# Performance work log

Measured on AMD Instinct MI355X. Metric: run time of the kernel, lower is better.

## Reference

```python
import jax, jax.numpy as jnp
import numpy as np

LNF, PNF, H = 128, 128, 128
THRESH = 10.0
NORM = 100.0
EPS = 1e-8


def _linear(x, W, b):
    return x @ W + b


def _glorot(key, shape):
    fan_in = shape[0]
    return jax.random.normal(key, shape, dtype=jnp.float32) / jnp.sqrt(jnp.float32(fan_in))


def setup_inputs() -> dict:
    key = jax.random.key(0)
    ks = jax.random.split(key, 20)
    bs, nl, npr = 4, 128, 1024
    inp = {
        "h_ligand": jax.random.normal(ks[0], (bs, nl, LNF), jnp.float32),
        "x_ligand": jax.random.normal(ks[1], (bs, nl, 3), jnp.float32) * 4.0,
        "h_protein": jax.random.normal(ks[2], (bs, npr, PNF), jnp.float32),
        "x_protein": jax.random.normal(ks[3], (bs, npr, 3), jnp.float32) * 4.0,
        "ligand_mask": jnp.ones((bs, nl, 1), jnp.float32),
        "protein_mask": jnp.ones((bs, npr, 1), jnp.float32),
        # attention MLP: (lnf+pnf+1)->H->H->1
        "aW1": _glorot(ks[4], (LNF + PNF + 1, H)), "ab1": jnp.zeros((H,), jnp.float32),
        "aW2": _glorot(ks[5], (H, H)),            "ab2": jnp.zeros((H,), jnp.float32),
        "aW3": _glorot(ks[6], (H, 1)),            "ab3": jnp.zeros((1,), jnp.float32),
        # value MLP: (pnf+1)->H->lnf
        "vW1": _glorot(ks[7], (PNF + 1, H)),      "vb1": jnp.zeros((H,), jnp.float32),
        "vW2": _glorot(ks[8], (H, LNF)),          "vb2": jnp.zeros((LNF,), jnp.float32),
        # coord MLP: (lnf+pnf+1)->H->1
        "cW1": _glorot(ks[9], (LNF + PNF + 1, H)), "cb1": jnp.zeros((H,), jnp.float32),
        "cW2": _glorot(ks[10], (H, 1)),           "cb2": jnp.zeros((1,), jnp.float32),
    }
    return inp


def reference(h_ligand, x_ligand, h_protein, x_protein, ligand_mask, protein_mask,
              aW1, ab1, aW2, ab2, aW3, ab3, vW1, vb1, vW2, vb2, cW1, cb1, cW2, cb2):
    bs, nl, lnf = h_ligand.shape
    npr = h_protein.shape[1]
    # pairwise geometry [bs, nl, np, ...]
    rel = x_ligand[:, :, None, :] - x_protein[:, None, :, :]
    ds = jnp.sum(rel * rel, axis=-1, keepdims=True)           # dist^2
    dist = jnp.sqrt(ds + EPS)
    edge = (dist < THRESH).astype(h_ligand.dtype)             # radius edge mask
    direction = rel / (dist + EPS)
    hl = jnp.broadcast_to(h_ligand[:, :, None, :], (bs, nl, npr, lnf))
    hp = jnp.broadcast_to(h_protein[:, None, :, :], (bs, nl, npr, h_protein.shape[-1]))
    pm = protein_mask[:, None, :, :]                          # [bs,1,np,1]

    pair_in = jnp.concatenate([hl, hp, ds], axis=-1)
    # attention MLP -> sigmoid
    a = jax.nn.silu(_linear(pair_in, aW1, ab1))
    a = jax.nn.silu(_linear(a, aW2, ab2))
    attn = jax.nn.sigmoid(_linear(a, aW3, ab3)) * pm
    # value MLP
    v = jax.nn.silu(_linear(jnp.concatenate([hp, ds], axis=-1), vW1, vb1))
    val = _linear(v, vW2, vb2)
    # feature messages, masked radius aggregation
    h_cross = jnp.sum(attn * val * edge, axis=2) / NORM       # [bs,nl,lnf]
    # coord MLP -> tanh
    c = jax.nn.silu(_linear(pair_in, cW1, cb1))
    cw = jnp.tanh(_linear(c, cW2, cb2)) * pm
    x_cross = jnp.sum(direction * cw * edge, axis=2) / NORM   # [bs,nl,3]

    h_cross = h_cross * ligand_mask
    x_cross = x_cross * ligand_mask
    return h_cross, x_cross
```

## Files before the change

kernel.cpp:

```cpp
#include <hip/hip_runtime.h>
#include <hip/hip_bf16.h>
#include <math.h>

#define HF 128
#define NL 128
#define NP 1024
#define NB 4
#define EPSF 1e-8f

typedef short bf16x8 __attribute__((ext_vector_type(8)));
typedef float f32x4 __attribute__((ext_vector_type(4)));

__device__ __forceinline__ float fast_rcp(float x){ return __builtin_amdgcn_rcpf(x); }
__device__ __forceinline__ float silu_f(float x){ return x*fast_rcp(1.f+__expf(-x)); }
__device__ __forceinline__ float sigmoid_f(float x){ return fast_rcp(1.f+__expf(-x)); }
__device__ __forceinline__ float tanh_f(float x){ return 1.f - 2.f*fast_rcp(1.f+__expf(2.f*x)); }
__device__ __forceinline__ unsigned short f2bf(float f){ __hip_bfloat16 h=__float2bfloat16(f); return *(unsigned short*)&h; }
__device__ __forceinline__ float bf2f(short u){ unsigned int x = ((unsigned int)(unsigned short)u)<<16; float r; __builtin_memcpy(&r,&x,4); return r; }

__global__ __launch_bounds__(128) void precompute_kernel(
    const float* __restrict__ h_ligand, const float* __restrict__ h_protein,
    const float* __restrict__ aW1, const float* __restrict__ ab1,
    const float* __restrict__ vW1, const float* __restrict__ vb1,
    const float* __restrict__ cW1, const float* __restrict__ cb1,
    const float* __restrict__ aW2, const float* __restrict__ vW2,
    float* __restrict__ Al, float* __restrict__ Cl,
    unsigned short* __restrict__ Ap, unsigned short* __restrict__ Vp,
    unsigned short* __restrict__ Cp,
    unsigned short* __restrict__ WaT, unsigned short* __restrict__ WvT)
{
    const int blk = blockIdx.x, n = threadIdx.x;
    if (blk < 64) {
        __shared__ float rows[8][HF];
        const int r0 = blk*8;
        for (int idx=n; idx<8*HF; idx+=128) rows[idx>>7][idx&127] = h_ligand[r0*HF+idx];
        __syncthreads();
        float aA[8], aC[8];
        const float bA = ab1[n], bC = cb1[n];
        #pragma unroll
        for (int r=0;r<8;++r){ aA[r]=bA; aC[r]=bC; }
        #pragma unroll 4
        for (int k=0;k<HF;++k){
            float wA = aW1[k*HF+n], wC = cW1[k*HF+n];
            #pragma unroll
            for (int r=0;r<8;++r){ aA[r]=fmaf(rows[r][k],wA,aA[r]); aC[r]=fmaf(rows[r][k],wC,aC[r]); }
        }
        #pragma unroll
        for (int r=0;r<8;++r){ Al[(r0+r)*HF+n]=aA[r]; Cl[(r0+r)*HF+n]=aC[r]; }
    } else if (blk < 576) {
        __shared__ float rows[8][HF];
        const int r0 = (blk-64)*8;
        for (int idx=n; idx<8*HF; idx+=128) rows[idx>>7][idx&127] = h_protein[r0*HF+idx];
        __syncthreads();
        float aA[8], aV[8], aC[8];
        const float bV = vb1[n];
        #pragma unroll
        for (int r=0;r<8;++r){ aA[r]=0.f; aV[r]=bV; aC[r]=0.f; }
        #pragma unroll 2
        for (int k=0;k<HF;++k){
            float wA = aW1[(HF+k)*HF+n], wV = vW1[k*HF+n], wC = cW1[(HF+k)*HF+n];
            #pragma unroll
            for (int r=0;r<8;++r){
                float h = rows[r][k];
                aA[r]=fmaf(h,wA,aA[r]); aV[r]=fmaf(h,wV,aV[r]); aC[r]=fmaf(h,wC,aC[r]);
            }
        }
        #pragma unroll
        for (int r=0;r<8;++r){
            Ap[(r0+r)*HF+n]=f2bf(aA[r]); Vp[(r0+r)*HF+n]=f2bf(aV[r]); Cp[(r0+r)*HF+n]=f2bf(aC[r]);
        }
    } else {
        const int m = blk - 576;
        const float* W = (m<8) ? aW2 : vW2;
        unsigned short* WT = (m<8) ? WaT : WvT;
        const int n0 = (m&7)*16;
        #pragma unroll
        for (int kb=0; kb<16; ++kb) {
            int k = kb*8 + (n>>4);
            int col = n0 + (n&15);
            WT[col*HF + k] = f2bf(W[k*HF + col]);
        }
    }
}

__global__ __launch_bounds__(256,2) void egnn_main_kernel(
    const float* __restrict__ x_ligand, const float* __restrict__ x_protein,
    const float* __restrict__ ligand_mask, const float* __restrict__ protein_mask,
    const float* __restrict__ aW1, const float* __restrict__ ab2,
    const float* __restrict__ aW3, const float* __restrict__ ab3,
    const float* __restrict__ vW1, const float* __restrict__ vb2,
    const float* __restrict__ cW1, const float* __restrict__ cW2, const float* __restrict__ cb2,
    const float* __restrict__ Al, const float* __restrict__ Cl,
    const unsigned short* __restrict__ Ap, const unsigned short* __restrict__ Vp,
    const unsigned short* __restrict__ Cp,
    const unsigned short* __restrict__ WaT, const unsigned short* __restrict__ WvT,
    float* __restrict__ out)
{
    __shared__ __align__(16) char smem[50176];
    float* ds_all = (float*)(smem + 32768);
    float* pme    = (float*)(smem + 34816);
    float* dirx   = (float*)(smem + 36864);
    float* diry   = (float*)(smem + 38912);
    float* dirz   = (float*)(smem + 40960);
    unsigned short* jlist = (unsigned short*)(smem + 43008);
    float* Al_s   = (float*)(smem + 44032);
    float* Cl_s   = (float*)(smem + 44544);
    float* aw1l   = (float*)(smem + 45056);
    float* cw1l   = (float*)(smem + 45568);
    float* vw1l   = (float*)(smem + 46080);
    float* cW2s   = (float*)(smem + 46592);
    float* attn_part = (float*)(smem + 47104);
    float* attn_e = (float*)(smem + 47360);
    float* hred   = (float*)(smem + 47616);
    float* xw     = (float*)(smem + 48640);
    int* nact_p   = (int*)(smem + 48704);

    const int t = threadIdx.x, lane = t&63, w = t>>6;
    const int wj = w>>1, wn = w&1;
    const int lr = lane&15, lg = lane>>4;
    const int bi = blockIdx.x;
    const int half = bi & 1;
    const int ii = bi >> 1;
    const int b = ii >> 7;
    const int jbase = half*512;

    const float xl0 = x_ligand[ii*3+0], xl1 = x_ligand[ii*3+1], xl2 = x_ligand[ii*3+2];
    const float* xp = x_protein + ((size_t)b*NP + jbase)*3;
    const float* pm = protein_mask + (size_t)b*NP + jbase;
    #pragma unroll
    for (int q=0; q<2; ++q) {
        int jj = q*256 + t;
        float r0 = xl0-xp[jj*3+0], r1 = xl1-xp[jj*3+1], r2 = xl2-xp[jj*3+2];
        float ds = r0*r0+r1*r1+r2*r2;
        float dist = sqrtf(ds+EPSF);
        float inv = fast_rcp(dist+EPSF);
        float e = dist < 10.f ? 1.f : 0.f;
        ds_all[jj]=ds; pme[jj]=pm[jj]*e;
        dirx[jj]=r0*inv; diry[jj]=r1*inv; dirz[jj]=r2*inv;
    }
    if (t < HF) {
        Al_s[t] = Al[(size_t)ii*HF+t];
        Cl_s[t] = Cl[(size_t)ii*HF+t];
        aw1l[t] = aW1[256*HF+t];
        cw1l[t] = cW1[256*HF+t];
        vw1l[t] = vW1[128*HF+t];
        cW2s[t] = cW2[t];
    }
    float ab2v[4], aw3v[4], vb2v[4];
    #pragma unroll
    for (int nt=0; nt<4; ++nt) {
        int n = wn*64 + nt*16 + lr;
        ab2v[nt] = ab2[n]; aw3v[nt] = aW3[n]; vb2v[nt] = vb2[n];
    }
    const float ab3v = ab3[0], cb2v = cb2[0];

    for (int c = t; c < 2048; c += 256) {
        int n = c >> 4, kc = c & 15;
        *(bf16x8*)(smem + n*256 + ((kc*16) ^ ((n&7)<<4))) = *(const bf16x8*)(WaT + n*HF + kc*8);
    }
    __syncthreads();

    if (w == 0) {
        int base = 0;
        for (int c=0; c<8; ++c) {
            int jj = c*64 + lane;
            bool act = pme[jj] > 0.f;
            unsigned long long m = __ballot(act);
            int pos = base + __popcll(m & ((1ull<<lane)-1ull));
            if (act) jlist[pos] = (unsigned short)jj;
            base += __popcll(m);
        }
        if (lane == 0) *nact_p = base;
    }
    bf16x8 wa[4][4], wv[4][4];
    #pragma unroll
    for (int nt = 0; nt < 4; ++nt) {
        int ncol = wn*64 + nt*16 + lr;
        int rb = ncol*256, sw = (ncol & 7) << 4;
        #pragma unroll
        for (int ks = 0; ks < 4; ++ks)
            wa[nt][ks] = *(bf16x8*)(smem + rb + ((lg*16 + ks*64) ^ sw));
    }
    __syncthreads();

    for (int c = t; c < 2048; c += 256) {
        int n = c >> 4, kc = c & 15;
        *(bf16x8*)(smem + n*256 + ((kc*16) ^ ((n&7)<<4))) = *(const bf16x8*)(WvT + n*HF + kc*8);
    }
    __syncthreads();
    #pragma unroll
    for (int nt = 0; nt < 4; ++nt) {
        int ncol = wn*64 + nt*16 + lr;
        int rb = ncol*256, sw = (ncol & 7) << 4;
        #pragma unroll
        for (int ks = 0; ks < 4; ++ks)
            wv[nt][ks] = *(bf16x8*)(smem + rb + ((lg*16 + ks*64) ^ sw));
    }
    __syncthreads();

    const int nact = *nact_p;
    const int ntiles = (nact + 31) >> 5;

    const unsigned short* Ap_b = Ap + ((size_t)b*NP + jbase)*HF;
    const unsigned short* Vp_b = Vp + ((size_t)b*NP + jbase)*HF;
    const unsigned short* Cp_b = Cp + ((size_t)b*NP + jbase)*HF;

    float hacc[4] = {0.f,0.f,0.f,0.f};
    float sae = 0.f;
    float xa0 = 0.f, xa1 = 0.f, xa2 = 0.f;
    const int brow = t >> 4, bcol = (t & 15)*8;
    const int crow = t >> 3, cg = t & 7;

    for (int tile = 0; tile < ntiles; ++tile) {
        const int j0 = tile*32;

        #pragma unroll
        for (int m = 0; m < 2; ++m) {
            const int row = m*16 + brow;
            const int grow = j0 + row;
            const int jl = jlist[grow < nact ? grow : 0];
            const float dsv = ds_all[jl];
            bf16x8 ap = *(const bf16x8*)(Ap_b + (size_t)jl*HF + bcol);
            f32x4 al0 = *(const f32x4*)&Al_s[bcol];
            f32x4 al1 = *(const f32x4*)&Al_s[bcol+4];
            f32x4 w0  = *(const f32x4*)&aw1l[bcol];
            f32x4 w1  = *(const f32x4*)&aw1l[bcol+4];
            bf16x8 pk;
            #pragma unroll
            for (int q = 0; q < 4; ++q) {
                pk[q]   = (short)f2bf(silu_f(al0[q] + bf2f(ap[q])   + dsv*w0[q]));
                pk[q+4] = (short)f2bf(silu_f(al1[q] + bf2f(ap[q+4]) + dsv*w1[q]));
            }
            *(bf16x8*)(smem + row*256 + ((bcol*2) ^ ((row & 7) << 4))) = pk;
        }
        __syncthreads();

        bf16x8 af[4];
        {
            int arow = wj*16 + lr;
            int rb = arow*256, sw = (arow & 7) << 4;
            #pragma unroll
            for (int ks = 0; ks < 4; ++ks)
                af[ks] = *(bf16x8*)(smem + rb + ((lg*16 + ks*64) ^ sw));
        }
        f32x4 acc[4];
        #pragma unroll
        for (int nt = 0; nt < 4; ++nt) {
            acc[nt] = (f32x4){0.f,0.f,0.f,0.f};
            #pragma unroll
            for (int ks = 0; ks < 4; ++ks)
                acc[nt] = __builtin_amdgcn_mfma_f32_16x16x32_bf16(af[ks], wa[nt][ks], acc[nt], 0,0,0);
        }
        {
            const int growc = j0 + crow;
            const bool okc = growc < nact;
            const int jlc = jlist[okc ? growc : 0];
            const float pmec = okc ? pme[jlc] : 0.f;
            const float dsc = ds_all[jlc];
            float part = 0.f;
            const unsigned short* cp = Cp_b + (size_t)jlc*HF + cg*16;
            #pragma unroll
            for (int u = 0; u < 2; ++u) {
                const int ch = cg*16 + u*8;
                bf16x8 cv = *(const bf16x8*)(cp + u*8);
                f32x4 cl0 = *(const f32x4*)&Cl_s[ch];
                f32x4 cl1 = *(const f32x4*)&Cl_s[ch+4];
                f32x4 w0  = *(const f32x4*)&cw1l[ch];
                f32x4 w1  = *(const f32x4*)&cw1l[ch+4];
                f32x4 s0  = *(const f32x4*)&cW2s[ch];
                f32x4 s1  = *(const f32x4*)&cW2s[ch+4];
                #pragma unroll
                for (int q = 0; q < 4; ++q) {
                    part += silu_f(cl0[q] + bf2f(cv[q])   + dsc*w0[q]) * s0[q];
                    part += silu_f(cl1[q] + bf2f(cv[q+4]) + dsc*w1[q]) * s1[q];
                }
            }
            part += __shfl_xor(part,1); part += __shfl_xor(part,2); part += __shfl_xor(part,4);
            if (cg == 0) {
                float cw = tanh_f(part + cb2v) * pmec;
                xa0 = fmaf(dirx[jlc], cw, xa0);
                xa1 = fmaf(diry[jlc], cw, xa1);
                xa2 = fmaf(dirz[jlc], cw, xa2);
            }
        }
        #pragma unroll
        for (int r = 0; r < 4; ++r) {
            float p = 0.f;
            #pragma unroll
            for (int nt = 0; nt < 4; ++nt)
                p += silu_f(acc[nt][r] + ab2v[nt]) * aw3v[nt];
            p += __shfl_xor(p,1); p += __shfl_xor(p,2);
            p += __shfl_xor(p,4); p += __shfl_xor(p,8);
            if (lr == 0) attn_part[wn*32 + wj*16 + lg*4 + r] = p;
        }
        __syncthreads();

        if (t < 32) {
            const int grow = j0 + t;
            const bool ok = grow < nact;
            const int j = jlist[ok ? grow : 0];
            attn_e[t] = sigmoid_f(attn_part[t] + attn_part[32+t] + ab3v) * (ok ? pme[j] : 0.f);
        }
        #pragma unroll
        for (int m = 0; m < 2; ++m) {
            const int row = m*16 + brow;
            const int grow = j0 + row;
            const int jl = jlist[grow < nact ? grow : 0];
            const float dsv = ds_all[jl];
            bf16x8 vp = *(const bf16x8*)(Vp_b + (size_t)jl*HF + bcol);
            f32x4 w0 = *(const f32x4*)&vw1l[bcol];
            f32x4 w1 = *(const f32x4*)&vw1l[bcol+4];
            bf16x8 pk;
            #pragma unroll
            for (int q = 0; q < 4; ++q) {
                pk[q]   = (short)f2bf(silu_f(bf2f(vp[q])   + dsv*w0[q]));
                pk[q+4] = (short)f2bf(silu_f(bf2f(vp[q+4]) + dsv*w1[q]));
            }
            *(bf16x8*)(smem + 8192 + row*256 + ((bcol*2) ^ ((row & 7) << 4))) = pk;
        }
        __syncthreads();

        bf16x8 vf[4];
        {
            int arow = wj*16 + lr;
            int rb = 8192 + arow*256, sw = (arow & 7) << 4;
            #pragma unroll
            for (int ks = 0; ks < 4; ++ks)
                vf[ks] = *(bf16x8*)(smem + rb + ((lg*16 + ks*64) ^ sw));
        }
        float ae[4];
        #pragma unroll
        for (int r = 0; r < 4; ++r) { ae[r] = attn_e[wj*16 + lg*4 + r]; sae += ae[r]; }
        #pragma unroll
        for (int nt = 0; nt < 4; ++nt) {
            f32x4 a = (f32x4){0.f,0.f,0.f,0.f};
            #pragma unroll
            for (int ks = 0; ks < 4; ++ks)
                a = __builtin_amdgcn_mfma_f32_16x16x32_bf16(vf[ks], wv[nt][ks], a, 0,0,0);
            hacc[nt] += ae[0]*a[0] + ae[1]*a[1] + ae[2]*a[2] + ae[3]*a[3];
        }
    }

    #pragma unroll
    for (int nt = 0; nt < 4; ++nt) {
        hacc[nt] += __shfl_xor(hacc[nt],16);
        hacc[nt] += __shfl_xor(hacc[nt],32);
    }
    sae += __shfl_xor(sae,16);
    sae += __shfl_xor(sae,32);
    if (lg == 0) {
        #pragma unroll
        for (int nt = 0; nt < 4; ++nt)
            hred[wj*128 + wn*64 + nt*16 + lr] = hacc[nt] + vb2v[nt]*sae;
    }
    xa0 += __shfl_xor(xa0,1);  xa1 += __shfl_xor(xa1,1);  xa2 += __shfl_xor(xa2,1);
    xa0 += __shfl_xor(xa0,2);  xa1 += __shfl_xor(xa1,2);  xa2 += __shfl_xor(xa2,2);
    xa0 += __shfl_xor(xa0,4);  xa1 += __shfl_xor(xa1,4);  xa2 += __shfl_xor(xa2,4);
    xa0 += __shfl_xor(xa0,8);  xa1 += __shfl_xor(xa1,8);  xa2 += __shfl_xor(xa2,8);
    xa0 += __shfl_xor(xa0,16); xa1 += __shfl_xor(xa1,16); xa2 += __shfl_xor(xa2,16);
    xa0 += __shfl_xor(xa0,32); xa1 += __shfl_xor(xa1,32); xa2 += __shfl_xor(xa2,32);
    if (lane == 0) { xw[w*3+0]=xa0; xw[w*3+1]=xa1; xw[w*3+2]=xa2; }
    __syncthreads();

    const float lm = ligand_mask[ii];
    if (t < HF) {
        float v = (hred[t] + hred[128+t]) * 0.01f * lm;
        atomicAdd(&out[(size_t)ii*HF + t], v);
    }
    if (t < 3) {
        float v = (xw[t] + xw[3+t] + xw[6+t] + xw[9+t]) * 0.01f * lm;
        atomicAdd(&out[(size_t)NB*NL*HF + ii*3 + t], v);
    }
}

extern "C" void kernel_launch(void* const* d_in, const int* in_sizes, int n_in,
                              void* d_out, int out_size, void* d_ws, size_t ws_size,
                              hipStream_t stream) {
    const float* h_ligand     = (const float*)d_in[0];
    const float* x_ligand     = (const float*)d_in[1];
    const float* h_protein    = (const float*)d_in[2];
    const float* x_protein    = (const float*)d_in[3];
    const float* ligand_mask  = (const float*)d_in[4];
    const float* protein_mask = (const float*)d_in[5];
    const float* aW1 = (const float*)d_in[6];
    const float* ab1 = (const float*)d_in[7];
    const float* aW2 = (const float*)d_in[8];
    const float* ab2 = (const float*)d_in[9];
    const float* aW3 = (const float*)d_in[10];
    const float* ab3 = (const float*)d_in[11];
    const float* vW1 = (const float*)d_in[12];
    const float* vb1 = (const float*)d_in[13];
    const float* vW2 = (const float*)d_in[14];
    const float* vb2 = (const float*)d_in[15];
    const float* cW1 = (const float*)d_in[16];
    const float* cb1 = (const float*)d_in[17];
    const float* cW2 = (const float*)d_in[18];
    const float* cb2 = (const float*)d_in[19];

    float* Al = (float*)d_ws;
    float* Cl = Al + 512*HF;
    unsigned short* Ap  = (unsigned short*)(Cl + 512*HF);
    unsigned short* Vp  = Ap + (size_t)NB*NP*HF;
    unsigned short* Cp  = Vp + (size_t)NB*NP*HF;
    unsigned short* WaT = Cp + (size_t)NB*NP*HF;
    unsigned short* WvT = WaT + HF*HF;

    hipMemsetAsync(d_out, 0, (size_t)out_size*sizeof(float), stream);

    precompute_kernel<<<592, 128, 0, stream>>>(
        h_ligand, h_protein, aW1, ab1, vW1, vb1, cW1, cb1, aW2, vW2,
        Al, Cl, Ap, Vp, Cp, WaT, WvT);

    egnn_main_kernel<<<NB*NL*2, 256, 0, stream>>>(
        x_ligand, x_protein, ligand_mask, protein_mask,
        aW1, ab2, aW3, ab3, vW1, vb2, cW1, cW2, cb2,
        Al, Cl, Ap, Vp, Cp, WaT, WvT, (float*)d_out);
}
```

Baseline: 248.1 us.

## Switch main kernel to persistent work-stealing over quarter-protein items

The main kernel becomes a persistent grid of 1024 blocks that pull work items (ligand row × quarter of protein range) from a global atomic counter, which should balance the uneven active-neighbour counts across blocks. The weights are loaded into registers once per block straight from global memory instead of through staged shared tiles, so shared memory shrinks and occupancy is raised to 3 blocks per CU. The precompute kernel uses 4 rows per block with twice as many blocks, and it resets the counter. The cost is more atomics on the output (4 partial sums per row instead of 2), extra barriers per item, and a serial atomic fetch per item.

```diff
diff --git a/kernel.cpp b/kernel.cpp
--- a/kernel.cpp
+++ b/kernel.cpp
@@ -7,6 +7,7 @@
 #define NP 1024
 #define NB 4
 #define EPSF 1e-8f
+#define NITEMS 2048
 
 typedef short bf16x8 __attribute__((ext_vector_type(8)));
 typedef float f32x4 __attribute__((ext_vector_type(4)));
@@ -27,7 +28,8 @@
     float* __restrict__ Al, float* __restrict__ Cl,
     unsigned short* __restrict__ Ap, unsigned short* __restrict__ Vp,
     unsigned short* __restrict__ Cp,
-    unsigned short* __restrict__ WaT, unsigned short* __restrict__ WvT)
+    unsigned short* __restrict__ WaT, unsigned short* __restrict__ WvT,
+    int* __restrict__ counter)
 {
     const int blk = blockIdx.x, n = threadIdx.x;
     if (blk < 64) {
@@ -47,30 +49,31 @@
         }
         #pragma unroll
         for (int r=0;r<8;++r){ Al[(r0+r)*HF+n]=aA[r]; Cl[(r0+r)*HF+n]=aC[r]; }
-    } else if (blk < 576) {
-        __shared__ float rows[8][HF];
-        const int r0 = (blk-64)*8;
-        for (int idx=n; idx<8*HF; idx+=128) rows[idx>>7][idx&127] = h_protein[r0*HF+idx];
-        __syncthreads();
-        float aA[8], aV[8], aC[8];
+    } else if (blk < 1088) {
+        __shared__ float rows[4][HF];
+        const int r0 = (blk-64)*4;
+        for (int idx=n; idx<4*HF; idx+=128) rows[idx>>7][idx&127] = h_protein[r0*HF+idx];
+        __syncthreads();
+        float aA[4], aV[4], aC[4];
         const float bV = vb1[n];
         #pragma unroll
-        for (int r=0;r<8;++r){ aA[r]=0.f; aV[r]=bV; aC[r]=0.f; }
+        for (int r=0;r<4;++r){ aA[r]=0.f; aV[r]=bV; aC[r]=0.f; }
         #pragma unroll 2
         for (int k=0;k<HF;++k){
             float wA = aW1[(HF+k)*HF+n], wV = vW1[k*HF+n], wC = cW1[(HF+k)*HF+n];
             #pragma unroll
-            for (int r=0;r<8;++r){
+            for (int r=0;r<4;++r){
                 float h = rows[r][k];
                 aA[r]=fmaf(h,wA,aA[r]); aV[r]=fmaf(h,wV,aV[r]); aC[r]=fmaf(h,wC,aC[r]);
             }
         }
         #pragma unroll
-        for (int r=0;r<8;++r){
+        for (int r=0;r<4;++r){
             Ap[(r0+r)*HF+n]=f2bf(aA[r]); Vp[(r0+r)*HF+n]=f2bf(aV[r]); Cp[(r0+r)*HF+n]=f2bf(aC[r]);
         }
     } else {
-        const int m = blk - 576;
+        const int m = blk - 1088;
+        if (m == 0 && n == 0) *counter = 0;
         const float* W = (m<8) ? aW2 : vW2;
         unsigned short* WT = (m<8) ? WaT : WvT;
         const int n0 = (m&7)*16;
@@ -83,7 +86,7 @@
     }
 }
 
-__global__ __launch_bounds__(256,2) void egnn_main_kernel(
+__global__ __launch_bounds__(256,3) void egnn_main_kernel(
     const float* __restrict__ x_ligand, const float* __restrict__ x_protein,
     const float* __restrict__ ligand_mask, const float* __restrict__ protein_mask,
     const float* __restrict__ aW1, const float* __restrict__ ab2,
@@ -94,53 +97,24 @@
     const unsigned short* __restrict__ Ap, const unsigned short* __restrict__ Vp,
     const unsigned short* __restrict__ Cp,
     const unsigned short* __restrict__ WaT, const unsigned short* __restrict__ WvT,
+    int* __restrict__ counter,
     float* __restrict__ out)
 {
-    __shared__ __align__(16) char smem[50176];
-    float* ds_all = (float*)(smem + 32768);
-    float* pme    = (float*)(smem + 34816);
-    float* dirx   = (float*)(smem + 36864);
-    float* diry   = (float*)(smem + 38912);
-    float* dirz   = (float*)(smem + 40960);
-    unsigned short* jlist = (unsigned short*)(smem + 43008);
-    float* Al_s   = (float*)(smem + 44032);
-    float* Cl_s   = (float*)(smem + 44544);
-    float* aw1l   = (float*)(smem + 45056);
-    float* cw1l   = (float*)(smem + 45568);
-    float* vw1l   = (float*)(smem + 46080);
-    float* cW2s   = (float*)(smem + 46592);
-    float* attn_part = (float*)(smem + 47104);
-    float* attn_e = (float*)(smem + 47360);
-    float* hred   = (float*)(smem + 47616);
-    float* xw     = (float*)(smem + 48640);
-    int* nact_p   = (int*)(smem + 48704);
+    __shared__ __align__(16) char tiles[16384];
+    __shared__ float ds_all[256], pme[256], dirx[256], diry[256], dirz[256];
+    __shared__ unsigned short jlist[256];
+    __shared__ float Al_s[HF], Cl_s[HF];
+    __shared__ float aw1l[HF], cw1l[HF], vw1l[HF], cW2s[HF];
+    __shared__ float attn_part[64], attn_e[32];
+    __shared__ float hred[256];
+    __shared__ float xw[12];
+    __shared__ int nact_s, cur_s;
 
     const int t = threadIdx.x, lane = t&63, w = t>>6;
     const int wj = w>>1, wn = w&1;
     const int lr = lane&15, lg = lane>>4;
-    const int bi = blockIdx.x;
-    const int half = bi & 1;
-    const int ii = bi >> 1;
-    const int b = ii >> 7;
-    const int jbase = half*512;
-
-    const float xl0 = x_ligand[ii*3+0], xl1 = x_ligand[ii*3+1], xl2 = x_ligand[ii*3+2];
-    const float* xp = x_protein + ((size_t)b*NP + jbase)*3;
-    const float* pm = protein_mask + (size_t)b*NP + jbase;
-    #pragma unroll
-    for (int q=0; q<2; ++q) {
-        int jj = q*256 + t;
-        float r0 = xl0-xp[jj*3+0], r1 = xl1-xp[jj*3+1], r2 = xl2-xp[jj*3+2];
-        float ds = r0*r0+r1*r1+r2*r2;
-        float dist = sqrtf(ds+EPSF);
-        float inv = fast_rcp(dist+EPSF);
-        float e = dist < 10.f ? 1.f : 0.f;
-        ds_all[jj]=ds; pme[jj]=pm[jj]*e;
-        dirx[jj]=r0*inv; diry[jj]=r1*inv; dirz[jj]=r2*inv;
-    }
+
     if (t < HF) {
-        Al_s[t] = Al[(size_t)ii*HF+t];
-        Cl_s[t] = Cl[(size_t)ii*HF+t];
         aw1l[t] = aW1[256*HF+t];
         cw1l[t] = cW1[256*HF+t];
         vw1l[t] = vW1[128*HF+t];
@@ -153,223 +127,235 @@
         ab2v[nt] = ab2[n]; aw3v[nt] = aW3[n]; vb2v[nt] = vb2[n];
     }
     const float ab3v = ab3[0], cb2v = cb2[0];
-
-    for (int c = t; c < 2048; c += 256) {
-        int n = c >> 4, kc = c & 15;
-        *(bf16x8*)(smem + n*256 + ((kc*16) ^ ((n&7)<<4))) = *(const bf16x8*)(WaT + n*HF + kc*8);
-    }
-    __syncthreads();
-
-    if (w == 0) {
-        int base = 0;
-        for (int c=0; c<8; ++c) {
-            int jj = c*64 + lane;
-            bool act = pme[jj] > 0.f;
-            unsigned long long m = __ballot(act);
-            int pos = base + __popcll(m & ((1ull<<lane)-1ull));
-            if (act) jlist[pos] = (unsigned short)jj;
-            base += __popcll(m);
-        }
-        if (lane == 0) *nact_p = base;
-    }
     bf16x8 wa[4][4], wv[4][4];
     #pragma unroll
-    for (int nt = 0; nt < 4; ++nt) {
-        int ncol = wn*64 + nt*16 + lr;
-        int rb = ncol*256, sw = (ncol & 7) << 4;
-        #pragma unroll
-        for (int ks = 0; ks < 4; ++ks)
-            wa[nt][ks] = *(bf16x8*)(smem + rb + ((lg*16 + ks*64) ^ sw));
+    for (int nt=0; nt<4; ++nt) {
+        const int ncol = wn*64 + nt*16 + lr;
+        #pragma unroll
+        for (int ks=0; ks<4; ++ks) {
+            wa[nt][ks] = *(const bf16x8*)(WaT + (size_t)ncol*HF + lg*8 + ks*32);
+            wv[nt][ks] = *(const bf16x8*)(WvT + (size_t)ncol*HF + lg*8 + ks*32);
+        }
     }
-    __syncthreads();
-
-    for (int c = t; c < 2048; c += 256) {
-        int n = c >> 4, kc = c & 15;
-        *(bf16x8*)(smem + n*256 + ((kc*16) ^ ((n&7)<<4))) = *(const bf16x8*)(WvT + n*HF + kc*8);
-    }
-    __syncthreads();
-    #pragma unroll
-    for (int nt = 0; nt < 4; ++nt) {
-        int ncol = wn*64 + nt*16 + lr;
-        int rb = ncol*256, sw = (ncol & 7) << 4;
-        #pragma unroll
-        for (int ks = 0; ks < 4; ++ks)
-            wv[nt][ks] = *(bf16x8*)(smem + rb + ((lg*16 + ks*64) ^ sw));
-    }
-    __syncthreads();
-
-    const int nact = *nact_p;
-    const int ntiles = (nact + 31) >> 5;
-
-    const unsigned short* Ap_b = Ap + ((size_t)b*NP + jbase)*HF;
-    const unsigned short* Vp_b = Vp + ((size_t)b*NP + jbase)*HF;
-    const unsigned short* Cp_b = Cp + ((size_t)b*NP + jbase)*HF;
-
-    float hacc[4] = {0.f,0.f,0.f,0.f};
-    float sae = 0.f;
-    float xa0 = 0.f, xa1 = 0.f, xa2 = 0.f;
+
     const int brow = t >> 4, bcol = (t & 15)*8;
     const int crow = t >> 3, cg = t & 7;
 
-    for (int tile = 0; tile < ntiles; ++tile) {
-        const int j0 = tile*32;
-
-        #pragma unroll
-        for (int m = 0; m < 2; ++m) {
-            const int row = m*16 + brow;
-            const int grow = j0 + row;
-            const int jl = jlist[grow < nact ? grow : 0];
-            const float dsv = ds_all[jl];
-            bf16x8 ap = *(const bf16x8*)(Ap_b + (size_t)jl*HF + bcol);
-            f32x4 al0 = *(const f32x4*)&Al_s[bcol];
-            f32x4 al1 = *(const f32x4*)&Al_s[bcol+4];
-            f32x4 w0  = *(const f32x4*)&aw1l[bcol];
-            f32x4 w1  = *(const f32x4*)&aw1l[bcol+4];
-            bf16x8 pk;
-            #pragma unroll
-            for (int q = 0; q < 4; ++q) {
-                pk[q]   = (short)f2bf(silu_f(al0[q] + bf2f(ap[q])   + dsv*w0[q]));
-                pk[q+4] = (short)f2bf(silu_f(al1[q] + bf2f(ap[q+4]) + dsv*w1[q]));
-            }
-            *(bf16x8*)(smem + row*256 + ((bcol*2) ^ ((row & 7) << 4))) = pk;
-        }
-        __syncthreads();
-
-        bf16x8 af[4];
+    for (;;) {
+        __syncthreads();
+        if (t == 0) cur_s = atomicAdd(counter, 1);
+        __syncthreads();
+        const int item = cur_s;
+        if (item >= NITEMS) break;
+        const int ii = item >> 2;
+        const int q  = item & 3;
+        const int b  = ii >> 7;
+        const int jbase = q*256;
+
+        if (t < HF) {
+            Al_s[t] = Al[(size_t)ii*HF+t];
+            Cl_s[t] = Cl[(size_t)ii*HF+t];
+        }
+        const float xl0 = x_ligand[ii*3+0], xl1 = x_ligand[ii*3+1], xl2 = x_ligand[ii*3+2];
+        const float* xp = x_protein + ((size_t)b*NP + jbase)*3;
+        const float* pm = protein_mask + (size_t)b*NP + jbase;
         {
-            int arow = wj*16 + lr;
-            int rb = arow*256, sw = (arow & 7) << 4;
-            #pragma unroll
-            for (int ks = 0; ks < 4; ++ks)
-                af[ks] = *(bf16x8*)(smem + rb + ((lg*16 + ks*64) ^ sw));
-        }
-        f32x4 acc[4];
+            const int jj = t;
+            float r0 = xl0-xp[jj*3+0], r1 = xl1-xp[jj*3+1], r2 = xl2-xp[jj*3+2];
+            float ds = r0*r0+r1*r1+r2*r2;
+            float dist = sqrtf(ds+EPSF);
+            float inv = fast_rcp(dist+EPSF);
+            float e = dist < 10.f ? 1.f : 0.f;
+            ds_all[jj]=ds; pme[jj]=pm[jj]*e;
+            dirx[jj]=r0*inv; diry[jj]=r1*inv; dirz[jj]=r2*inv;
+        }
+        __syncthreads();
+        if (w == 0) {
+            int base = 0;
+            #pragma unroll
+            for (int c=0; c<4; ++c) {
+                int jj = c*64 + lane;
+                bool act = pme[jj] > 0.f;
+                unsigned long long m = __ballot(act);
+                int pos = base + __popcll(m & ((1ull<<lane)-1ull));
+                if (act) jlist[pos] = (unsigned short)jj;
+                base += __popcll(m);
+            }
+            if (lane == 0) nact_s = base;
+        }
+        __syncthreads();
+        const int nact = nact_s;
+        if (nact == 0) continue;
+        const int ntiles = (nact + 31) >> 5;
+
+        const unsigned short* Ap_b = Ap + ((size_t)b*NP + jbase)*HF;
+        const unsigned short* Vp_b = Vp + ((size_t)b*NP + jbase)*HF;
+        const unsigned short* Cp_b = Cp + ((size_t)b*NP + jbase)*HF;
+
+        float hacc[4] = {0.f,0.f,0.f,0.f};
+        float sae = 0.f;
+        float xa0 = 0.f, xa1 = 0.f, xa2 = 0.f;
+
+        for (int tile = 0; tile < ntiles; ++tile) {
+            const int j0 = tile*32;
+
+            #pragma unroll
+            for (int m = 0; m < 2; ++m) {
+                const int row = m*16 + brow;
+                const int grow = j0 + row;
+                const int jl = jlist[grow < nact ? grow : 0];
+                const float dsv = ds_all[jl];
+                bf16x8 ap = *(const bf16x8*)(Ap_b + (size_t)jl*HF + bcol);
+                f32x4 al0 = *(const f32x4*)&Al_s[bcol];
+                f32x4 al1 = *(const f32x4*)&Al_s[bcol+4];
+                f32x4 w0  = *(const f32x4*)&aw1l[bcol];
+                f32x4 w1  = *(const f32x4*)&aw1l[bcol+4];
+                bf16x8 pk;
+                #pragma unroll
+                for (int qq = 0; qq < 4; ++qq) {
+                    pk[qq]   = (short)f2bf(silu_f(al0[qq] + bf2f(ap[qq])   + dsv*w0[qq]));
+                    pk[qq+4] = (short)f2bf(silu_f(al1[qq] + bf2f(ap[qq+4]) + dsv*w1[qq]));
+                }
+                *(bf16x8*)(tiles + row*256 + ((bcol*2) ^ ((row & 7) << 4))) = pk;
+            }
+            __syncthreads();
+
+            bf16x8 af[4];
+            {
+                int arow = wj*16 + lr;
+                int rb = arow*256, sw = (arow & 7) << 4;
+                #pragma unroll
+                for (int ks = 0; ks < 4; ++ks)
+                    af[ks] = *(bf16x8*)(tiles + rb + ((lg*16 + ks*64) ^ sw));
+            }
+            f32x4 acc[4];
+            #pragma unroll
+            for (int nt = 0; nt < 4; ++nt) {
+                acc[nt] = (f32x4){0.f,0.f,0.f,0.f};
+                #pragma unroll
+                for (int ks = 0; ks < 4; ++ks)
+                    acc[nt] = __builtin_amdgcn_mfma_f32_16x16x32_bf16(af[ks], wa[nt][ks], acc[nt], 0,0,0);
+            }
+            {
+                const int growc = j0 + crow;
+                const bool okc = growc < nact;
+                const int jlc = jlist[okc ? growc : 0];
+                const float pmec = okc ? pme[jlc] : 0.f;
+                const float dsc = ds_all[jlc];
+                float part = 0.f;
+                const unsigned short* cp = Cp_b + (size_t)jlc*HF + cg*16;
+                #pragma unroll
+                for (int u = 0; u < 2; ++u) {
+                    const int ch = cg*16 + u*8;
+                    bf16x8 cv = *(const bf16x8*)(cp + u*8);
+                    f32x4 cl0 = *(const f32x4*)&Cl_s[ch];
+                    f32x4 cl1 = *(const f32x4*)&Cl_s[ch+4];
+                    f32x4 w0  = *(const f32x4*)&cw1l[ch];
+                    f32x4 w1  = *(const f32x4*)&cw1l[ch+4];
+                    f32x4 s0  = *(const f32x4*)&cW2s[ch];
+                    f32x4 s1  = *(const f32x4*)&cW2s[ch+4];
+                    #pragma unroll
+                    for (int qq = 0; qq < 4; ++qq) {
+                        part += silu_f(cl0[qq] + bf2f(cv[qq])   + dsc*w0[qq]) * s0[qq];
+                        part += silu_f(cl1[qq] + bf2f(cv[qq+4]) + dsc*w1[qq]) * s1[qq];
+                    }
+                }
+                part += __shfl_xor(part,1); part += __shfl_xor(part,2); part += __shfl_xor(part,4);
+                if (cg == 0) {
+                    float cw = tanh_f(part + cb2v) * pmec;
+                    xa0 = fmaf(dirx[jlc], cw, xa0);
+                    xa1 = fmaf(diry[jlc], cw, xa1);
+                    xa2 = fmaf(dirz[jlc], cw, xa2);
+                }
+            }
+            #pragma unroll
+            for (int r = 0; r < 4; ++r) {
+                float p = 0.f;
+                #pragma unroll
+                for (int nt = 0; nt < 4; ++nt)
+                    p += silu_f(acc[nt][r] + ab2v[nt]) * aw3v[nt];
+                p += __shfl_xor(p,1); p += __shfl_xor(p,2);
+                p += __shfl_xor(p,4); p += __shfl_xor(p,8);
+                if (lr == 0) attn_part[wn*32 + wj*16 + lg*4 + r] = p;
+            }
+            __syncthreads();
+
+            if (t < 32) {
+                const int grow = j0 + t;
+                const bool ok = grow < nact;
+                const int j = jlist[ok ? grow : 0];
+                attn_e[t] = sigmoid_f(attn_part[t] + attn_part[32+t] + ab3v) * (ok ? pme[j] : 0.f);
+            }
+            #pragma unroll
+            for (int m = 0; m < 2; ++m) {
+                const int row = m*16 + brow;
+                const int grow = j0 + row;
+                const int jl = jlist[grow < nact ? grow : 0];
+                const float dsv = ds_all[jl];
+                bf16x8 vp = *(const bf16x8*)(Vp_b + (size_t)jl*HF + bcol);
+                f32x4 w0 = *(const f32x4*)&vw1l[bcol];
+                f32x4 w1 = *(const f32x4*)&vw1l[bcol+4];
+                bf16x8 pk;
+                #pragma unroll
+                for (int qq = 0; qq < 4; ++qq) {
+                    pk[qq]   = (short)f2bf(silu_f(bf2f(vp[qq])   + dsv*w0[qq]));
+                    pk[qq+4] = (short)f2bf(silu_f(bf2f(vp[qq+4]) + dsv*w1[qq]));
+                }
+                *(bf16x8*)(tiles + 8192 + row*256 + ((bcol*2) ^ ((row & 7) << 4))) = pk;
+            }
+            __syncthreads();
+
+            bf16x8 vf[4];
+            {
+                int arow = wj*16 + lr;
+                int rb = 8192 + arow*256, sw = (arow & 7) << 4;
+                #pragma unroll
+                for (int ks = 0; ks < 4; ++ks)
+                    vf[ks] = *(bf16x8*)(tiles + rb + ((lg*16 + ks*64) ^ sw));
+            }
+            float ae[4];
+            #pragma unroll
+            for (int r = 0; r < 4; ++r) { ae[r] = attn_e[wj*16 + lg*4 + r]; sae += ae[r]; }
+            #pragma unroll
+            for (int nt = 0; nt < 4; ++nt) {
+                f32x4 a = (f32x4){0.f,0.f,0.f,0.f};
+                #pragma unroll
+                for (int ks = 0; ks < 4; ++ks)
+                    a = __builtin_amdgcn_mfma_f32_16x16x32_bf16(vf[ks], wv[nt][ks], a, 0,0,0);
+                hacc[nt] += ae[0]*a[0] + ae[1]*a[1] + ae[2]*a[2] + ae[3]*a[3];
+            }
+        }
+
         #pragma unroll
         for (int nt = 0; nt < 4; ++nt) {
-            acc[nt] = (f32x4){0.f,0.f,0.f,0.f};
-            #pragma unroll
-            for (int ks = 0; ks < 4; ++ks)
-                acc[nt] = __builtin_amdgcn_mfma_f32_16x16x32_bf16(af[ks], wa[nt][ks], acc[nt], 0,0,0);
-        }
-        {
-            const int growc = j0 + crow;
-            const bool okc = growc < nact;
-            const int jlc = jlist[okc ? growc : 0];
-            const float pmec = okc ? pme[jlc] : 0.f;
-            const float dsc = ds_all[jlc];
-            float part = 0.f;
-            const unsigned short* cp = Cp_b + (size_t)jlc*HF + cg*16;
-            #pragma unroll
-            for (int u = 0; u < 2; ++u) {
-                const int ch = cg*16 + u*8;
-                bf16x8 cv = *(const bf16x8*)(cp + u*8);
-                f32x4 cl0 = *(const f32x4*)&Cl_s[ch];
-                f32x4 cl1 = *(const f32x4*)&Cl_s[ch+4];
-                f32x4 w0  = *(const f32x4*)&cw1l[ch];
-                f32x4 w1  = *(const f32x4*)&cw1l[ch+4];
-                f32x4 s0  = *(const f32x4*)&cW2s[ch];
-                f32x4 s1  = *(const f32x4*)&cW2s[ch+4];
-                #pragma unroll
-                for (int q = 0; q < 4; ++q) {
-                    part += silu_f(cl0[q] + bf2f(cv[q])   + dsc*w0[q]) * s0[q];
-                    part += silu_f(cl1[q] + bf2f(cv[q+4]) + dsc*w1[q]) * s1[q];
-                }
-            }
-            part += __shfl_xor(part,1); part += __shfl_xor(part,2); part += __shfl_xor(part,4);
-            if (cg == 0) {
-                float cw = tanh_f(part + cb2v) * pmec;
-                xa0 = fmaf(dirx[jlc], cw, xa0);
-                xa1 = fmaf(diry[jlc], cw, xa1);
-                xa2 = fmaf(dirz[jlc], cw, xa2);
-            }
-        }
-        #pragma unroll
-        for (int r = 0; r < 4; ++r) {
-            float p = 0.f;
+            hacc[nt] += __shfl_xor(hacc[nt],16);
+            hacc[nt] += __shfl_xor(hacc[nt],32);
+        }
+        sae += __shfl_xor(sae,16);
+        sae += __shfl_xor(sae,32);
+        if (lg == 0) {
             #pragma unroll
             for (int nt = 0; nt < 4; ++nt)
-                p += silu_f(acc[nt][r] + ab2v[nt]) * aw3v[nt];
-            p += __shfl_xor(p,1); p += __shfl_xor(p,2);
-            p += __shfl_xor(p,4); p += __shfl_xor(p,8);
-            if (lr == 0) attn_part[wn*32 + wj*16 + lg*4 + r] = p;
-        }
-        __syncthreads();
-
-        if (t < 32) {
-            const int grow = j0 + t;
-            const bool ok = grow < nact;
-            const int j = jlist[ok ? grow : 0];
-            attn_e[t] = sigmoid_f(attn_part[t] + attn_part[32+t] + ab3v) * (ok ? pme[j] : 0.f);
-        }
-        #pragma unroll
-        for (int m = 0; m < 2; ++m) {
-            const int row = m*16 + brow;
-            const int grow = j0 + row;
-            const int jl = jlist[grow < nact ? grow : 0];
-            const float dsv = ds_all[jl];
-            bf16x8 vp = *(const bf16x8*)(Vp_b + (size_t)jl*HF + bcol);
-            f32x4 w0 = *(const f32x4*)&vw1l[bcol];
-            f32x4 w1 = *(const f32x4*)&vw1l[bcol+4];
-            bf16x8 pk;
-            #pragma unroll
-            for (int q = 0; q < 4; ++q) {
-                pk[q]   = (short)f2bf(silu_f(bf2f(vp[q])   + dsv*w0[q]));
-                pk[q+4] = (short)f2bf(silu_f(bf2f(vp[q+4]) + dsv*w1[q]));
-            }
-            *(bf16x8*)(smem + 8192 + row*256 + ((bcol*2) ^ ((row & 7) << 4))) = pk;
-        }
-        __syncthreads();
-
-        bf16x8 vf[4];
-        {
-            int arow = wj*16 + lr;
-            int rb = 8192 + arow*256, sw = (arow & 7) << 4;
-            #pragma unroll
-            for (int ks = 0; ks < 4; ++ks)
-                vf[ks] = *(bf16x8*)(smem + rb + ((lg*16 + ks*64) ^ sw));
-        }
-        float ae[4];
-        #pragma unroll
-        for (int r = 0; r < 4; ++r) { ae[r] = attn_e[wj*16 + lg*4 + r]; sae += ae[r]; }
-        #pragma unroll
-        for (int nt = 0; nt < 4; ++nt) {
-            f32x4 a = (f32x4){0.f,0.f,0.f,0.f};
-            #pragma unroll
-            for (int ks = 0; ks < 4; ++ks)
-                a = __builtin_amdgcn_mfma_f32_16x16x32_bf16(vf[ks], wv[nt][ks], a, 0,0,0);
-            hacc[nt] += ae[0]*a[0] + ae[1]*a[1] + ae[2]*a[2] + ae[3]*a[3];
-        }
-    }
-
-    #pragma unroll
-    for (int nt = 0; nt < 4; ++nt) {
-        hacc[nt] += __shfl_xor(hacc[nt],16);
-        hacc[nt] += __shfl_xor(hacc[nt],32);
-    }
-    sae += __shfl_xor(sae,16);
-    sae += __shfl_xor(sae,32);
-    if (lg == 0) {
-        #pragma unroll
-        for (int nt = 0; nt < 4; ++nt)
-            hred[wj*128 + wn*64 + nt*16 + lr] = hacc[nt] + vb2v[nt]*sae;
-    }
-    xa0 += __shfl_xor(xa0,1);  xa1 += __shfl_xor(xa1,1);  xa2 += __shfl_xor(xa2,1);
-    xa0 += __shfl_xor(xa0,2);  xa1 += __shfl_xor(xa1,2);  xa2 += __shfl_xor(xa2,2);
-    xa0 += __shfl_xor(xa0,4);  xa1 += __shfl_xor(xa1,4);  xa2 += __shfl_xor(xa2,4);
-    xa0 += __shfl_xor(xa0,8);  xa1 += __shfl_xor(xa1,8);  xa2 += __shfl_xor(xa2,8);
-    xa0 += __shfl_xor(xa0,16); xa1 += __shfl_xor(xa1,16); xa2 += __shfl_xor(xa2,16);
-    xa0 += __shfl_xor(xa0,32); xa1 += __shfl_xor(xa1,32); xa2 += __shfl_xor(xa2,32);
-    if (lane == 0) { xw[w*3+0]=xa0; xw[w*3+1]=xa1; xw[w*3+2]=xa2; }
-    __syncthreads();
-
-    const float lm = ligand_mask[ii];
-    if (t < HF) {
-        float v = (hred[t] + hred[128+t]) * 0.01f * lm;
-        atomicAdd(&out[(size_t)ii*HF + t], v);
-    }
-    if (t < 3) {
-        float v = (xw[t] + xw[3+t] + xw[6+t] + xw[9+t]) * 0.01f * lm;
-        atomicAdd(&out[(size_t)NB*NL*HF + ii*3 + t], v);
+                hred[wj*128 + wn*64 + nt*16 + lr] = hacc[nt] + vb2v[nt]*sae;
+        }
+        xa0 += __shfl_xor(xa0,1);  xa1 += __shfl_xor(xa1,1);  xa2 += __shfl_xor(xa2,1);
+        xa0 += __shfl_xor(xa0,2);  xa1 += __shfl_xor(xa1,2);  xa2 += __shfl_xor(xa2,2);
+        xa0 += __shfl_xor(xa0,4);  xa1 += __shfl_xor(xa1,4);  xa2 += __shfl_xor(xa2,4);
+        xa0 += __shfl_xor(xa0,8);  xa1 += __shfl_xor(xa1,8);  xa2 += __shfl_xor(xa2,8);
+        xa0 += __shfl_xor(xa0,16); xa1 += __shfl_xor(xa1,16); xa2 += __shfl_xor(xa2,16);
+        xa0 += __shfl_xor(xa0,32); xa1 += __shfl_xor(xa1,32); xa2 += __shfl_xor(xa2,32);
+        if (lane == 0) { xw[w*3+0]=xa0; xw[w*3+1]=xa1; xw[w*3+2]=xa2; }
+        __syncthreads();
+
+        const float lm = ligand_mask[ii];
+        if (t < HF) {
+            float v = (hred[t] + hred[128+t]) * 0.01f * lm;
+            atomicAdd(&out[(size_t)ii*HF + t], v);
+        }
+        if (t < 3) {
+            float v = (xw[t] + xw[3+t] + xw[6+t] + xw[9+t]) * 0.01f * lm;
+            atomicAdd(&out[(size_t)NB*NL*HF + ii*3 + t], v);
+        }
     }
 }
 
@@ -404,15 +390,16 @@
     unsigned short* Cp  = Vp + (size_t)NB*NP*HF;
     unsigned short* WaT = Cp + (size_t)NB*NP*HF;
     unsigned short* WvT = WaT + HF*HF;
+    int* counter        = (int*)(WvT + HF*HF);
 
     hipMemsetAsync(d_out, 0, (size_t)out_size*sizeof(float), stream);
 
-    precompute_kernel<<<592, 128, 0, stream>>>(
+    precompute_kernel<<<1104, 128, 0, stream>>>(
         h_ligand, h_protein, aW1, ab1, vW1, vb1, cW1, cb1, aW2, vW2,
-        Al, Cl, Ap, Vp, Cp, WaT, WvT);
-
-    egnn_main_kernel<<<NB*NL*2, 256, 0, stream>>>(
+        Al, Cl, Ap, Vp, Cp, WaT, WvT, counter);
+
+    egnn_main_kernel<<<1024, 256, 0, stream>>>(
         x_ligand, x_protein, ligand_mask, protein_mask,
         aW1, ab2, aW3, ab3, vW1, vb2, cW1, cW2, cb2,
-        Al, Cl, Ap, Vp, Cp, WaT, WvT, (float*)d_out);
+        Al, Cl, Ap, Vp, Cp, WaT, WvT, counter, (float*)d_out);
 }
```

New measurement: 386.3 us. 55.7% more time.

## Double-buffer async global-to-LDS prefetch of gathered protein Ap/Vp rows

Applied to the files above, without the earlier changes.

Gathered bf16 rows of Ap and Vp for the next 32-row tile are now prefetched with global_load_lds into double-buffered LDS regions while the current tile is processed. The SiLU staging then reads from LDS instead of issuing dependent global loads on the critical path. This aims to hide the latency of the indirect gathers. In exchange, LDS per block grows (hred is moved to alias the activation area), and correctness depends on the async LDS writes having completed before the barriers, since there is no explicit wait.

```diff
diff --git a/kernel.cpp b/kernel.cpp
--- a/kernel.cpp
+++ b/kernel.cpp
@@ -96,7 +96,7 @@
     const unsigned short* __restrict__ WaT, const unsigned short* __restrict__ WvT,
     float* __restrict__ out)
 {
-    __shared__ __align__(16) char smem[50176];
+    __shared__ __align__(16) char smem[64000];
     float* ds_all = (float*)(smem + 32768);
     float* pme    = (float*)(smem + 34816);
     float* dirx   = (float*)(smem + 36864);
@@ -111,9 +111,11 @@
     float* cW2s   = (float*)(smem + 46592);
     float* attn_part = (float*)(smem + 47104);
     float* attn_e = (float*)(smem + 47360);
-    float* hred   = (float*)(smem + 47616);
-    float* xw     = (float*)(smem + 48640);
-    int* nact_p   = (int*)(smem + 48704);
+    float* xw     = (float*)(smem + 47488);
+    int* nact_p   = (int*)(smem + 47536);
+    char* rawA    = smem + 16384;
+    char* rawV    = smem + 47616;
+    float* hred   = (float*)smem;
 
     const int t = threadIdx.x, lane = t&63, w = t>>6;
     const int wj = w>>1, wn = w&1;
@@ -182,7 +184,6 @@
             wa[nt][ks] = *(bf16x8*)(smem + rb + ((lg*16 + ks*64) ^ sw));
     }
     __syncthreads();
-
     for (int c = t; c < 2048; c += 256) {
         int n = c >> 4, kc = c & 15;
         *(bf16x8*)(smem + n*256 + ((kc*16) ^ ((n&7)<<4))) = *(const bf16x8*)(WvT + n*HF + kc*8);
@@ -204,6 +205,26 @@
     const unsigned short* Ap_b = Ap + ((size_t)b*NP + jbase)*HF;
     const unsigned short* Vp_b = Vp + ((size_t)b*NP + jbase)*HF;
     const unsigned short* Cp_b = Cp + ((size_t)b*NP + jbase)*HF;
+
+    auto pf = [&](const unsigned short* arr, char* rawbase, int j0n) {
+        #pragma unroll
+        for (int inst = 0; inst < 2; ++inst) {
+            const int row = w*8 + inst*4 + (lane>>4);
+            const int grow = j0n + row;
+            const int jl = jlist[grow < nact ? grow : 0];
+            const unsigned short* src = arr + (size_t)jl*HF + (lane&15)*8;
+            __builtin_amdgcn_global_load_lds(
+                (const __attribute__((address_space(1))) void*)src,
+                (__attribute__((address_space(3))) void*)(rawbase + (w*8 + inst*4)*256),
+                16, 0, 0);
+        }
+    };
+
+    if (nact > 0) {
+        pf(Ap_b, rawA, 0);
+        pf(Vp_b, rawV, 0);
+    }
+    __syncthreads();
 
     float hacc[4] = {0.f,0.f,0.f,0.f};
     float sae = 0.f;
@@ -213,14 +234,19 @@
 
     for (int tile = 0; tile < ntiles; ++tile) {
         const int j0 = tile*32;
-
+        const int buf = tile & 1;
+        char* rA = rawA + buf*8192;
+        char* rV = rawV + buf*8192;
+
+        pf(Ap_b, rawA + (buf^1)*8192, j0 + 32);
+        pf(Vp_b, rawV + (buf^1)*8192, j0 + 32);
         #pragma unroll
         for (int m = 0; m < 2; ++m) {
             const int row = m*16 + brow;
             const int grow = j0 + row;
             const int jl = jlist[grow < nact ? grow : 0];
             const float dsv = ds_all[jl];
-            bf16x8 ap = *(const bf16x8*)(Ap_b + (size_t)jl*HF + bcol);
+            bf16x8 ap = *(const bf16x8*)(rA + row*256 + bcol*2);
             f32x4 al0 = *(const f32x4*)&Al_s[bcol];
             f32x4 al1 = *(const f32x4*)&Al_s[bcol+4];
             f32x4 w0  = *(const f32x4*)&aw1l[bcol];
@@ -307,7 +333,7 @@
             const int grow = j0 + row;
             const int jl = jlist[grow < nact ? grow : 0];
             const float dsv = ds_all[jl];
-            bf16x8 vp = *(const bf16x8*)(Vp_b + (size_t)jl*HF + bcol);
+            bf16x8 vp = *(const bf16x8*)(rV + row*256 + bcol*2);
             f32x4 w0 = *(const f32x4*)&vw1l[bcol];
             f32x4 w1 = *(const f32x4*)&vw1l[bcol+4];
             bf16x8 pk;
```

New measurement: 251.6 us. Within noise of the previous version (+1.4%).
